# Kernel tuning notes

Measured on AMD Instinct MI355X. Metric: run time of the kernel, lower is better.

The kernel has to match this reference:

```python
import jax, jax.numpy as jnp
import numpy as np

N = 100000   # nodes per type
E = 800000   # edges per relation
D = 128      # hidden/out channels


def _sage(x_src, x_dst, src, dst, Wl, bl, Wr, n_dst):
    # PyG SAGEConv (mean aggr, bipartite): lin_l(mean_j x_src[j]) + lin_r(x_dst)
    msg = x_src[src]                                                    # [E, D] gather
    agg = jax.ops.segment_sum(msg, dst, num_segments=n_dst)            # [n_dst, D]
    cnt = jax.ops.segment_sum(jnp.ones((src.shape[0],), x_src.dtype), dst, num_segments=n_dst)
    mean = agg / jnp.maximum(cnt, 1.0)[:, None]
    return mean @ Wl.T + bl + x_dst @ Wr.T


def _metapath(xu, xi, ei0, ei1, Wl0, bl0, Wr0, Wl1, bl1, Wr1, outW, outb):
    # hop0: user -> item ; hop1: item -> user ; start_type = 'user'
    hi = jax.nn.relu(_sage(xu, xi, ei0[0], ei0[1], Wl0, bl0, Wr0, xi.shape[0]))
    hu = jax.nn.relu(_sage(hi, xu, ei1[0], ei1[1], Wl1, bl1, Wr1, xu.shape[0]))
    return hu @ outW.T + outb                                           # [N, D]


def setup_inputs() -> dict:
    key = jax.random.key(0)
    ks = jax.random.split(key, 32)
    s = 1.0 / np.sqrt(D)
    w = lambda k, shp: (jax.random.normal(k, shp, jnp.float32) * s)
    d = {
        'x_user': jax.random.normal(ks[0], (N, D), jnp.float32),
        'x_item': jax.random.normal(ks[1], (N, D), jnp.float32),
        'ei_m0_h0': jax.random.randint(ks[2], (2, E), 0, N),
        'ei_m0_h1': jax.random.randint(ks[3], (2, E), 0, N),
        'ei_m1_h0': jax.random.randint(ks[4], (2, E), 0, N),
        'ei_m1_h1': jax.random.randint(ks[5], (2, E), 0, N),
    }
    names = ['Wl_00', 'Wr_00', 'Wl_01', 'Wr_01', 'Wl_10', 'Wr_10', 'Wl_11', 'Wr_11', 'outW_0', 'outW_1']
    for i, nm in enumerate(names):
        d[nm] = w(ks[6 + i], (D, D))
    for nm in ['bl_00', 'bl_01', 'bl_10', 'bl_11', 'outb_0', 'outb_1']:
        d[nm] = jnp.zeros((D,), jnp.float32)
    d['regW'] = w(ks[20], (1, 2 * D))
    d['regb'] = jnp.zeros((1,), jnp.float32)
    return d


def reference(x_user, x_item, ei_m0_h0, ei_m0_h1, ei_m1_h0, ei_m1_h1,
              Wl_00, bl_00, Wr_00, Wl_01, bl_01, Wr_01,
              Wl_10, bl_10, Wr_10, Wl_11, bl_11, Wr_11,
              outW_0, outb_0, outW_1, outb_1, regW, regb):
    emb0 = _metapath(x_user, x_item, ei_m0_h0, ei_m0_h1,
                     Wl_00, bl_00, Wr_00, Wl_01, bl_01, Wr_01, outW_0, outb_0)
    emb1 = _metapath(x_user, x_item, ei_m1_h0, ei_m1_h1,
                     Wl_10, bl_10, Wr_10, Wl_11, bl_11, Wr_11, outW_1, outb_1)
    concat = jnp.concatenate([emb0, emb1], axis=-1)                     # [N, 2D]
    return (concat @ regW.T + regb).squeeze(-1)                         # [N]
```

## Files before the change

### kernel.cpp

```cpp
#include <hip/hip_runtime.h>

#define DIM 128
#define CHUNK 8192
#define PAIRC 4096
#define SENT 0xFFFFFFFFu
typedef unsigned short ushort_t;
typedef short bf16x8 __attribute__((ext_vector_type(8)));
typedef float f32x4 __attribute__((ext_vector_type(4)));

__device__ inline ushort_t f2bf(float f) {
    unsigned int u = __float_as_uint(f);
    unsigned int r = (u + 0x7FFFu + ((u >> 16) & 1u)) >> 16;
    return (ushort_t)r;
}
__device__ inline unsigned int pack2bf(float lo, float hi) {
    return (unsigned int)f2bf(lo) | ((unsigned int)f2bf(hi) << 16);
}
__device__ inline float bflo2f(unsigned int u) { return __uint_as_float(u << 16); }
__device__ inline float bfhi2f(unsigned int u) { return __uint_as_float(u & 0xFFFF0000u); }

__global__ void f32_to_bf16_kernel(const float* __restrict__ in, ushort_t* __restrict__ out, int n4) {
    int i = blockIdx.x * blockDim.x + threadIdx.x;
    int stride = gridDim.x * blockDim.x;
    for (; i < n4; i += stride) {
        float4 v = *reinterpret_cast<const float4*>(in + (size_t)i * 4);
        ushort_t o[4] = {f2bf(v.x), f2bf(v.y), f2bf(v.z), f2bf(v.w)};
        *reinterpret_cast<uint2*>(out + (size_t)i * 4) = *reinterpret_cast<uint2*>(o);
    }
}

__global__ void pack_weights_kernel(const float* __restrict__ Wl, const float* __restrict__ Wr,
                                    ushort_t* __restrict__ Wcat) {
    int j = blockIdx.x, k = threadIdx.x;
    float v = (k < DIM) ? Wl[j * DIM + k] : Wr[j * DIM + (k - DIM)];
    Wcat[j * 256 + k] = f2bf(v);
}

__global__ void precompute_v_kernel(const float* __restrict__ outW0,
                                    const float* __restrict__ outW1,
                                    const float* __restrict__ outb0,
                                    const float* __restrict__ outb1,
                                    const float* __restrict__ regW,
                                    const float* __restrict__ regb,
                                    float* __restrict__ vbuf) {
    int t = threadIdx.x;
    if (t < DIM) {
        float s = 0.f;
        #pragma unroll 8
        for (int j = 0; j < DIM; ++j) s = fmaf(outW0[j * DIM + t], regW[j], s);
        vbuf[t] = s;
    } else {
        int k = t - DIM;
        float s = 0.f;
        #pragma unroll 8
        for (int j = 0; j < DIM; ++j) s = fmaf(outW1[j * DIM + k], regW[DIM + j], s);
        vbuf[t] = s;
    }
    if (t == 0) {
        float c = regb[0];
        for (int j = 0; j < DIM; ++j) c += outb0[j] * regW[j] + outb1[j] * regW[DIM + j];
        vbuf[2 * DIM] = c;
    }
}

struct EdgePtrs { const int* e[4]; };

__global__ void bin4_direct_kernel(EdgePtrs eps, int nedges, int* __restrict__ bpad,
                                   int* __restrict__ breal,
                                   unsigned int* __restrict__ pairs, int nbuck) {
    int list = blockIdx.y;
    const int* __restrict__ src = eps.e[list];
    const int* __restrict__ dst = eps.e[list] + nedges;
    __shared__ int cnt[512], goff[512];
    const int tid = threadIdx.x;
    const int base = blockIdx.x * CHUNK;
    for (int b = tid; b < nbuck; b += 256) cnt[b] = 0;
    __syncthreads();
    int dstv[CHUNK / 256];
    #pragma unroll
    for (int it = 0; it < CHUNK / 256; ++it) {
        int e = base + it * 256 + tid;
        int d = (e < nedges) ? dst[e] : -1;
        dstv[it] = d;
        if (d >= 0) atomicAdd(&cnt[d >> 8], 1);
    }
    __syncthreads();
    for (int b = tid; b < nbuck; b += 256) {
        int c = cnt[b];
        int res = (c + 31) & ~31;
        int off = 0;
        if (res > 0) {
            off = atomicAdd(&bpad[list * nbuck + b], res);
            atomicAdd(&breal[list * nbuck + b], c);
            unsigned int* pb = pairs + ((size_t)list * nbuck + b) * PAIRC + off;
            for (int i = c; i < res; ++i) pb[i] = SENT;
        }
        goff[b] = off;
        cnt[b] = 0;
    }
    __syncthreads();
    #pragma unroll
    for (int it = 0; it < CHUNK / 256; ++it) {
        int d = dstv[it];
        if (d >= 0) {
            int e = base + it * 256 + tid;
            int b = d >> 8;
            int r = atomicAdd(&cnt[b], 1);
            pairs[((size_t)list * nbuck + b) * PAIRC + goff[b] + r] =
                ((unsigned int)src[e] << 8) | (unsigned int)(d & 255);
        }
    }
}

__global__ void bucket_scan_kernel(const int* __restrict__ breal, int* __restrict__ bbase,
                                   int n, int* __restrict__ rowptr, int n4, int total) {
    int t = threadIdx.x;
    int loc[4];
    int s = 0;
    #pragma unroll
    for (int k = 0; k < 4; ++k) {
        int i = t * 4 + k;
        loc[k] = (i < n) ? breal[i] : 0;
        s += loc[k];
    }
    int lane = t & 63, w = t >> 6;
    int sv = s;
    #pragma unroll
    for (int off = 1; off < 64; off <<= 1) {
        int u = __shfl_up(sv, off);
        if (lane >= off) sv += u;
    }
    __shared__ int wsum[8];
    if (lane == 63) wsum[w] = sv;
    __syncthreads();
    int base = 0;
    #pragma unroll
    for (int k = 0; k < 8; ++k)
        if (k < w) base += wsum[k];
    int ex = base + sv - s;
    #pragma unroll
    for (int k = 0; k < 4; ++k) {
        int i = t * 4 + k;
        if (i < n) bbase[i] = ex;
        ex += loc[k];
    }
    if (t == 0) rowptr[n4] = total;
}

__global__ void fillb_kernel(const unsigned int* __restrict__ pairs, const int* __restrict__ bpad,
                             const int* __restrict__ bbase, int* __restrict__ rowptr,
                             int* __restrict__ eidx, int N, int nbuck) {
    int list = blockIdx.y;
    int b = blockIdx.x;
    int d0 = b << 8;
    if (d0 >= N) return;
    int nd = N - d0; if (nd > 256) nd = 256;
    int slot = list * nbuck + b;
    int cntp = bpad[slot];
    int base = bbase[slot];
    const unsigned int* __restrict__ ps = pairs + (size_t)slot * PAIRC;

    __shared__ int h[256], cur[256];
    int t = threadIdx.x;
    h[t] = 0;
    __syncthreads();
    for (int i = t; i < cntp; i += 256) {
        unsigned int p = ps[i];
        if (p != SENT) atomicAdd(&h[p & 255u], 1);
    }
    __syncthreads();
    int v = h[t];
    int lane = t & 63, w = t >> 6;
    int sv = v;
    #pragma unroll
    for (int off = 1; off < 64; off <<= 1) {
        int u = __shfl_up(sv, off);
        if (lane >= off) sv += u;
    }
    __shared__ int wsum[4];
    if (lane == 63) wsum[w] = sv;
    __syncthreads();
    int wbase = 0;
    #pragma unroll
    for (int k = 0; k < 4; ++k)
        if (k < w) wbase += wsum[k];
    int ex = wbase + sv - v;
    if (t < nd) rowptr[(size_t)list * N + d0 + t] = base + ex;
    cur[t] = ex;
    __syncthreads();
    for (int i = t; i < cntp; i += 256) {
        unsigned int p = ps[i];
        if (p != SENT) {
            int ld = (int)(p & 255u);
            int r = atomicAdd(&cur[ld], 1);
            eidx[base + r] = (int)(p >> 8);
        }
    }
}

__global__ void aggregate_kernel(const ushort_t* __restrict__ xsrc,
                                 const int* __restrict__ rowptr,
                                 const int* __restrict__ eidx,
                                 ushort_t* __restrict__ mean, int n) {
    int wid = (blockIdx.x * blockDim.x + threadIdx.x) >> 6;
    int lane = threadIdx.x & 63;
    int nw = (gridDim.x * blockDim.x) >> 6;
    const int sub = lane >> 4;
    const int lr = lane & 15;
    for (int r = wid; r < n; r += nw) {
        int beg = rowptr[r];
        int end = rowptr[r + 1];
        int deg = end - beg;
        float a[8] = {0.f, 0.f, 0.f, 0.f, 0.f, 0.f, 0.f, 0.f};
        int nit = (deg + 3) >> 2;
        for (int it = 0; it < nit; ++it) {
            int j = beg + it * 4 + sub;
            if (j < end) {
                int s = eidx[j];
                uint4 u = *reinterpret_cast<const uint4*>(xsrc + (size_t)s * DIM + lr * 8);
                a[0] += bflo2f(u.x); a[1] += bfhi2f(u.x);
                a[2] += bflo2f(u.y); a[3] += bfhi2f(u.y);
                a[4] += bflo2f(u.z); a[5] += bfhi2f(u.z);
                a[6] += bflo2f(u.w); a[7] += bfhi2f(u.w);
            }
        }
        #pragma unroll
        for (int k = 0; k < 8; ++k) {
            a[k] += __shfl_xor(a[k], 16);
            a[k] += __shfl_xor(a[k], 32);
        }
        if (sub == 0) {
            float sc = 1.0f / fmaxf((float)deg, 1.0f);
            uint4 o;
            o.x = pack2bf(a[0] * sc, a[1] * sc);
            o.y = pack2bf(a[2] * sc, a[3] * sc);
            o.z = pack2bf(a[4] * sc, a[5] * sc);
            o.w = pack2bf(a[6] * sc, a[7] * sc);
            *reinterpret_cast<uint4*>(mean + (size_t)r * DIM + lr * 8) = o;
        }
    }
}

template <int MODE>
__launch_bounds__(256, 2)
__global__ void sage_gemm_mfma(const ushort_t* __restrict__ A0,
                               const ushort_t* __restrict__ A1,
                               const ushort_t* __restrict__ Wcat,
                               const float* __restrict__ bl,
                               ushort_t* __restrict__ H,
                               const float* __restrict__ v,
                               const float* __restrict__ cptr,
                               float* __restrict__ out,
                               int nrows) {
    __shared__ ushort_t As[128][40];
    __shared__ ushort_t Bs[128][40];
    __shared__ float red[2][128];

    const int tid = threadIdx.x;
    const int lane = tid & 63;
    const int w = tid >> 6;
    const int wr = w >> 1, wc = w & 1;
    const int lr = lane & 15;
    const int lk = (lane >> 4) * 8;
    const int row0 = blockIdx.x * 128;

    f32x4 acc[4][4];
    #pragma unroll
    for (int m = 0; m < 4; ++m)
        #pragma unroll
        for (int n = 0; n < 4; ++n)
            acc[m][n] = (f32x4){0.f, 0.f, 0.f, 0.f};

    for (int kt = 0; kt < 8; ++kt) {
        const int kb = kt * 32;
        const ushort_t* __restrict__ Asrc = (kb < DIM) ? A0 : A1;
        const int kbb = kb & (DIM - 1);

        #pragma unroll
        for (int p = 0; p < 2; ++p) {
            int idx = p * 256 + tid;
            int r = idx >> 2, c = idx & 3;
            int grow = row0 + r;
            uint4 val = make_uint4(0u, 0u, 0u, 0u);
            if (grow < nrows)
                val = *reinterpret_cast<const uint4*>(Asrc + (size_t)grow * DIM + kbb + c * 8);
            *reinterpret_cast<uint4*>(&As[r][c * 8]) = val;
        }
        #pragma unroll
        for (int p = 0; p < 2; ++p) {
            int idx = p * 256 + tid;
            int j = idx >> 2, c = idx & 3;
            uint4 val = *reinterpret_cast<const uint4*>(Wcat + j * 256 + kb + c * 8);
            *reinterpret_cast<uint4*>(&Bs[j][c * 8]) = val;
        }
        __syncthreads();

        bf16x8 af[4], bfm[4];
        #pragma unroll
        for (int m = 0; m < 4; ++m)
            af[m] = *reinterpret_cast<const bf16x8*>(&As[wr * 64 + m * 16 + lr][lk]);
        #pragma unroll
        for (int n = 0; n < 4; ++n)
            bfm[n] = *reinterpret_cast<const bf16x8*>(&Bs[wc * 64 + n * 16 + lr][lk]);
        #pragma unroll
        for (int m = 0; m < 4; ++m)
            #pragma unroll
            for (int n = 0; n < 4; ++n)
                acc[m][n] = __builtin_amdgcn_mfma_f32_16x16x32_bf16(af[m], bfm[n], acc[m][n], 0, 0, 0);
        __syncthreads();
    }

    if (MODE == 0) {
        float blc[4];
        #pragma unroll
        for (int n = 0; n < 4; ++n) blc[n] = bl[wc * 64 + n * 16 + lr];
        #pragma unroll
        for (int m = 0; m < 4; ++m) {
            #pragma unroll
            for (int reg = 0; reg < 4; ++reg) {
                int row = row0 + wr * 64 + m * 16 + (lane >> 4) * 4 + reg;
                if (row < nrows) {
                    #pragma unroll
                    for (int n = 0; n < 4; ++n) {
                        int col = wc * 64 + n * 16 + lr;
                        H[(size_t)row * DIM + col] = f2bf(fmaxf(acc[m][n][reg] + blc[n], 0.f));
                    }
                }
            }
        }
    } else {
        float blc[4], vc[4];
        #pragma unroll
        for (int n = 0; n < 4; ++n) {
            int col = wc * 64 + n * 16 + lr;
            blc[n] = bl[col];
            vc[n] = v[col];
        }
        #pragma unroll
        for (int m = 0; m < 4; ++m) {
            float rp[4] = {0.f, 0.f, 0.f, 0.f};
            #pragma unroll
            for (int n = 0; n < 4; ++n)
                #pragma unroll
                for (int reg = 0; reg < 4; ++reg)
                    rp[reg] = fmaf(fmaxf(acc[m][n][reg] + blc[n], 0.f), vc[n], rp[reg]);
            #pragma unroll
            for (int reg = 0; reg < 4; ++reg) {
                float p = rp[reg];
                p += __shfl_xor(p, 1);
                p += __shfl_xor(p, 2);
                p += __shfl_xor(p, 4);
                p += __shfl_xor(p, 8);
                if (lr == 0)
                    red[wc][wr * 64 + m * 16 + (lane >> 4) * 4 + reg] = p;
            }
        }
        __syncthreads();
        if (tid < 128) {
            int row = row0 + tid;
            if (row < nrows) {
                float s = red[0][tid] + red[1][tid];
                if (MODE == 1) out[row] = cptr[0] + s;
                else out[row] += s;
            }
        }
    }
}

extern "C" void kernel_launch(void* const* d_in, const int* in_sizes, int n_in,
                              void* d_out, int out_size, void* d_ws, size_t ws_size,
                              hipStream_t stream) {
    const float* x_user = (const float*)d_in[0];
    const float* x_item = (const float*)d_in[1];
    const int* ei_m0_h0 = (const int*)d_in[2];
    const int* ei_m0_h1 = (const int*)d_in[3];
    const int* ei_m1_h0 = (const int*)d_in[4];
    const int* ei_m1_h1 = (const int*)d_in[5];
    const float* Wl00 = (const float*)d_in[6];
    const float* Wr00 = (const float*)d_in[7];
    const float* Wl01 = (const float*)d_in[8];
    const float* Wr01 = (const float*)d_in[9];
    const float* Wl10 = (const float*)d_in[10];
    const float* Wr10 = (const float*)d_in[11];
    const float* Wl11 = (const float*)d_in[12];
    const float* Wr11 = (const float*)d_in[13];
    const float* outW0 = (const float*)d_in[14];
    const float* outW1 = (const float*)d_in[15];
    const float* bl00 = (const float*)d_in[16];
    const float* bl01 = (const float*)d_in[17];
    const float* bl10 = (const float*)d_in[18];
    const float* bl11 = (const float*)d_in[19];
    const float* outb0 = (const float*)d_in[20];
    const float* outb1 = (const float*)d_in[21];
    const float* regW = (const float*)d_in[22];
    const float* regb = (const float*)d_in[23];

    const int N = in_sizes[0] / DIM;
    const int E = in_sizes[2] / 2;
    float* out = (float*)d_out;

    const int n4 = 4 * N;
    const int nbuck = (N + 255) >> 8;
    ushort_t* xbu = (ushort_t*)d_ws;
    ushort_t* xbi = xbu + (size_t)N * DIM;
    ushort_t* meanb = xbi + (size_t)N * DIM;
    ushort_t* hib = meanb + (size_t)N * DIM;
    unsigned int* pairs = (unsigned int*)meanb;
    ushort_t* Wcat = hib + (size_t)N * DIM;
    float* vbuf = (float*)(Wcat + 4 * 128 * 256);
    int* bpad = (int*)(vbuf + 2 * DIM + 1);
    int* breal = bpad + 4 * nbuck;
    int* bbase = breal + 4 * nbuck;
    int* rowptr = bbase + 4 * nbuck;
    int* eidx = rowptr + n4 + 1;

    f32_to_bf16_kernel<<<2048, 256, 0, stream>>>(x_user, xbu, N * DIM / 4);
    f32_to_bf16_kernel<<<2048, 256, 0, stream>>>(x_item, xbi, N * DIM / 4);
    pack_weights_kernel<<<128, 256, 0, stream>>>(Wl00, Wr00, Wcat);
    pack_weights_kernel<<<128, 256, 0, stream>>>(Wl01, Wr01, Wcat + 1 * 32768);
    pack_weights_kernel<<<128, 256, 0, stream>>>(Wl10, Wr10, Wcat + 2 * 32768);
    pack_weights_kernel<<<128, 256, 0, stream>>>(Wl11, Wr11, Wcat + 3 * 32768);
    precompute_v_kernel<<<1, 256, 0, stream>>>(outW0, outW1, outb0, outb1, regW, regb, vbuf);

    EdgePtrs eps;
    eps.e[0] = ei_m0_h0; eps.e[1] = ei_m0_h1; eps.e[2] = ei_m1_h0; eps.e[3] = ei_m1_h1;
    hipMemsetAsync(bpad, 0, (size_t)8 * nbuck * sizeof(int), stream);
    bin4_direct_kernel<<<dim3((E + CHUNK - 1) / CHUNK, 4), 256, 0, stream>>>(eps, E, bpad, breal, pairs, nbuck);
    bucket_scan_kernel<<<1, 512, 0, stream>>>(breal, bbase, 4 * nbuck, rowptr, n4, 4 * E);
    fillb_kernel<<<dim3(nbuck, 4), 256, 0, stream>>>(pairs, bpad, bbase, rowptr, eidx, N, nbuck);

    const int gemmBlocks = (N + 127) / 128;
    const int aggBlocks = 2048;

    struct Hop {
        const ushort_t* xsrc;
        const ushort_t* xdst;
        const ushort_t* W;
        const float* bl;
        int mode;
        const float* v;
    };
    const Hop hops[4] = {
        {xbu, xbi, Wcat + 0 * 32768, bl00, 0, nullptr},
        {hib, xbu, Wcat + 1 * 32768, bl01, 1, vbuf},
        {xbu, xbi, Wcat + 2 * 32768, bl10, 0, nullptr},
        {hib, xbu, Wcat + 3 * 32768, bl11, 2, vbuf + DIM},
    };

    for (int h = 0; h < 4; ++h) {
        const Hop& hp = hops[h];
        aggregate_kernel<<<aggBlocks, 256, 0, stream>>>(hp.xsrc, rowptr + (size_t)h * N, eidx, meanb, N);
        if (hp.mode == 0)
            sage_gemm_mfma<0><<<gemmBlocks, 256, 0, stream>>>(meanb, hp.xdst, hp.W, hp.bl,
                                                              hib, nullptr, nullptr, nullptr, N);
        else if (hp.mode == 1)
            sage_gemm_mfma<1><<<gemmBlocks, 256, 0, stream>>>(meanb, hp.xdst, hp.W, hp.bl,
                                                              nullptr, hp.v, vbuf + 2 * DIM, out, N);
        else
            sage_gemm_mfma<2><<<gemmBlocks, 256, 0, stream>>>(meanb, hp.xdst, hp.W, hp.bl,
                                                              nullptr, hp.v, vbuf + 2 * DIM, out, N);
    }
}
```

Baseline: 376.1 us.

## Stage binned edge pairs in shared memory and merge small setup launches

The binning kernel now packs each chunk's edges into a shared-memory staging buffer laid out by bucket (prefix-scanned local offsets, padding reduced from 32 to 16). Each wave then copies whole buckets out contiguously, with sentinel padding, instead of scattering single pairs to global memory. The two bf16 conversions and the four weight-pack kernels are each merged into one launch to cut launch overhead. The trade-off is a large shared-memory footprint (about 56KB of staging) that lowers occupancy, and a fixed STAGECAP that assumes padded counts per chunk fit.

Result: no change. 373.2 us (-0.8%).

```diff
diff --git a/kernel.cpp b/kernel.cpp
--- a/kernel.cpp
+++ b/kernel.cpp
@@ -4,6 +4,7 @@
 #define CHUNK 8192
 #define PAIRC 4096
 #define SENT 0xFFFFFFFFu
+#define STAGECAP 14080
 typedef unsigned short ushort_t;
 typedef short bf16x8 __attribute__((ext_vector_type(8)));
 typedef float f32x4 __attribute__((ext_vector_type(4)));
@@ -19,7 +20,10 @@
 __device__ inline float bflo2f(unsigned int u) { return __uint_as_float(u << 16); }
 __device__ inline float bfhi2f(unsigned int u) { return __uint_as_float(u & 0xFFFF0000u); }
 
-__global__ void f32_to_bf16_kernel(const float* __restrict__ in, ushort_t* __restrict__ out, int n4) {
+__global__ void f32_to_bf16_2_kernel(const float* __restrict__ a, const float* __restrict__ b,
+                                     ushort_t* __restrict__ oa, ushort_t* __restrict__ ob, int n4) {
+    const float* __restrict__ in = blockIdx.y ? b : a;
+    ushort_t* __restrict__ out = blockIdx.y ? ob : oa;
     int i = blockIdx.x * blockDim.x + threadIdx.x;
     int stride = gridDim.x * blockDim.x;
     for (; i < n4; i += stride) {
@@ -29,11 +33,12 @@
     }
 }
 
-__global__ void pack_weights_kernel(const float* __restrict__ Wl, const float* __restrict__ Wr,
-                                    ushort_t* __restrict__ Wcat) {
-    int j = blockIdx.x, k = threadIdx.x;
-    float v = (k < DIM) ? Wl[j * DIM + k] : Wr[j * DIM + (k - DIM)];
-    Wcat[j * 256 + k] = f2bf(v);
+struct WPack { const float* Wl[4]; const float* Wr[4]; };
+
+__global__ void pack_weights4_kernel(WPack wp, ushort_t* __restrict__ Wcat) {
+    int l = blockIdx.y, j = blockIdx.x, k = threadIdx.x;
+    float v = (k < DIM) ? wp.Wl[l][j * DIM + k] : wp.Wr[l][j * DIM + (k - DIM)];
+    Wcat[l * 32768 + j * 256 + k] = f2bf(v);
 }
 
 __global__ void precompute_v_kernel(const float* __restrict__ outW0,
@@ -65,17 +70,22 @@
 
 struct EdgePtrs { const int* e[4]; };
 
-__global__ void bin4_direct_kernel(EdgePtrs eps, int nedges, int* __restrict__ bpad,
-                                   int* __restrict__ breal,
-                                   unsigned int* __restrict__ pairs, int nbuck) {
+__global__ void bin4_stage_kernel(EdgePtrs eps, int nedges, int* __restrict__ bpad,
+                                  int* __restrict__ breal,
+                                  unsigned int* __restrict__ pairs, int nbuck) {
     int list = blockIdx.y;
     const int* __restrict__ src = eps.e[list];
     const int* __restrict__ dst = eps.e[list] + nedges;
-    __shared__ int cnt[512], goff[512];
+    __shared__ int cnt[512], loff[512], goff[512];
+    __shared__ int wsum[4];
+    __shared__ unsigned int stage[STAGECAP];
     const int tid = threadIdx.x;
+    const int lane = tid & 63, w = tid >> 6;
     const int base = blockIdx.x * CHUNK;
-    for (int b = tid; b < nbuck; b += 256) cnt[b] = 0;
-    __syncthreads();
+
+    for (int b = tid; b < 512; b += 256) cnt[b] = 0;
+    __syncthreads();
+
     int dstv[CHUNK / 256];
     #pragma unroll
     for (int it = 0; it < CHUNK / 256; ++it) {
@@ -85,30 +95,58 @@
         if (d >= 0) atomicAdd(&cnt[d >> 8], 1);
     }
     __syncthreads();
+
+    {
+        int b0 = tid * 2, b1 = b0 + 1;
+        int r0 = (cnt[b0] + 15) & ~15;
+        int r1 = (cnt[b1] + 15) & ~15;
+        int s = r0 + r1;
+        int sv = s;
+        #pragma unroll
+        for (int off = 1; off < 64; off <<= 1) {
+            int u = __shfl_up(sv, off);
+            if (lane >= off) sv += u;
+        }
+        if (lane == 63) wsum[w] = sv;
+        __syncthreads();
+        int bw = 0;
+        #pragma unroll
+        for (int k = 0; k < 4; ++k)
+            if (k < w) bw += wsum[k];
+        int ex = bw + sv - s;
+        loff[b0] = ex;
+        loff[b1] = ex + r0;
+    }
     for (int b = tid; b < nbuck; b += 256) {
         int c = cnt[b];
-        int res = (c + 31) & ~31;
-        int off = 0;
+        int res = (c + 15) & ~15;
         if (res > 0) {
-            off = atomicAdd(&bpad[list * nbuck + b], res);
+            goff[b] = atomicAdd(&bpad[list * nbuck + b], res);
             atomicAdd(&breal[list * nbuck + b], c);
-            unsigned int* pb = pairs + ((size_t)list * nbuck + b) * PAIRC + off;
-            for (int i = c; i < res; ++i) pb[i] = SENT;
-        }
-        goff[b] = off;
+        }
         cnt[b] = 0;
     }
     __syncthreads();
+
     #pragma unroll
     for (int it = 0; it < CHUNK / 256; ++it) {
         int d = dstv[it];
         if (d >= 0) {
             int e = base + it * 256 + tid;
-            int b = d >> 8;
-            int r = atomicAdd(&cnt[b], 1);
-            pairs[((size_t)list * nbuck + b) * PAIRC + goff[b] + r] =
-                ((unsigned int)src[e] << 8) | (unsigned int)(d & 255);
-        }
+            int r = atomicAdd(&cnt[d >> 8], 1);
+            stage[loff[d >> 8] + r] = ((unsigned int)src[e] << 8) | (unsigned int)(d & 255);
+        }
+    }
+    __syncthreads();
+
+    for (int b = w; b < nbuck; b += 4) {
+        int c = cnt[b];
+        int res = (c + 15) & ~15;
+        if (res == 0) continue;
+        size_t go = ((size_t)list * nbuck + b) * PAIRC + goff[b];
+        int lo = loff[b];
+        for (int i = lane; i < res; i += 64)
+            pairs[go + i] = (i < c) ? stage[lo + i] : SENT;
     }
 }
 
@@ -414,18 +452,17 @@
     int* rowptr = bbase + 4 * nbuck;
     int* eidx = rowptr + n4 + 1;
 
-    f32_to_bf16_kernel<<<2048, 256, 0, stream>>>(x_user, xbu, N * DIM / 4);
-    f32_to_bf16_kernel<<<2048, 256, 0, stream>>>(x_item, xbi, N * DIM / 4);
-    pack_weights_kernel<<<128, 256, 0, stream>>>(Wl00, Wr00, Wcat);
-    pack_weights_kernel<<<128, 256, 0, stream>>>(Wl01, Wr01, Wcat + 1 * 32768);
-    pack_weights_kernel<<<128, 256, 0, stream>>>(Wl10, Wr10, Wcat + 2 * 32768);
-    pack_weights_kernel<<<128, 256, 0, stream>>>(Wl11, Wr11, Wcat + 3 * 32768);
+    f32_to_bf16_2_kernel<<<dim3(1024, 2), 256, 0, stream>>>(x_user, x_item, xbu, xbi, N * DIM / 4);
+    WPack wp;
+    wp.Wl[0] = Wl00; wp.Wl[1] = Wl01; wp.Wl[2] = Wl10; wp.Wl[3] = Wl11;
+    wp.Wr[0] = Wr00; wp.Wr[1] = Wr01; wp.Wr[2] = Wr10; wp.Wr[3] = Wr11;
+    pack_weights4_kernel<<<dim3(128, 4), 256, 0, stream>>>(wp, Wcat);
     precompute_v_kernel<<<1, 256, 0, stream>>>(outW0, outW1, outb0, outb1, regW, regb, vbuf);
 
     EdgePtrs eps;
     eps.e[0] = ei_m0_h0; eps.e[1] = ei_m0_h1; eps.e[2] = ei_m1_h0; eps.e[3] = ei_m1_h1;
     hipMemsetAsync(bpad, 0, (size_t)8 * nbuck * sizeof(int), stream);
-    bin4_direct_kernel<<<dim3((E + CHUNK - 1) / CHUNK, 4), 256, 0, stream>>>(eps, E, bpad, breal, pairs, nbuck);
+    bin4_stage_kernel<<<dim3((E + CHUNK - 1) / CHUNK, 4), 256, 0, stream>>>(eps, E, bpad, breal, pairs, nbuck);
     bucket_scan_kernel<<<1, 512, 0, stream>>>(breal, bbase, 4 * nbuck, rowptr, n4, 4 * E);
     fillb_kernel<<<dim3(nbuck, 4), 256, 0, stream>>>(pairs, bpad, bbase, rowptr, eidx, N, nbuck);
 
```
